# Kernel tuning notes

Hardware: AMD Instinct MI355X
Metric: run time of the kernel (lower is better)

## Reference

```python
import jax, jax.numpy as jnp
import numpy as np

N = 100000      # nodes
E = 1600000     # edges (avg degree 16)
F_IN = 128      # num_node_features
H = 128         # hidden_size
C = 64          # num_classes


def sage_conv(x, src, dst, W_l, W_r, b, num_nodes):
    """PyG SAGEConv (mean aggr): out = lin_l(mean_{j->i} x_j) + lin_r(x_i) + b."""
    msg = x[src]                                                  # [E, F] gather
    agg = jax.ops.segment_sum(msg, dst, num_segments=num_nodes)   # [N, F] scatter-add
    deg = jax.ops.segment_sum(jnp.ones((src.shape[0],), x.dtype), dst,
                              num_segments=num_nodes)             # [N]
    agg = agg / jnp.maximum(deg, 1.0)[:, None]                    # mean (safe for isolated nodes)
    return agg @ W_l + x @ W_r + b


def setup_inputs() -> dict:
    key = jax.random.key(0)
    ks = jax.random.split(key, 8)
    x = jax.random.normal(ks[0], (N, F_IN), dtype=jnp.float32)
    edge_index = jax.random.randint(ks[1], (2, E), 0, N, dtype=jnp.int32).astype(jnp.int64)
    W1_l = jax.random.normal(ks[2], (F_IN, H), dtype=jnp.float32) / np.float32(np.sqrt(F_IN))
    W1_r = jax.random.normal(ks[3], (F_IN, H), dtype=jnp.float32) / np.float32(np.sqrt(F_IN))
    b1 = jnp.zeros((H,), jnp.float32)
    W2_l = jax.random.normal(ks[4], (H, C), dtype=jnp.float32) / np.float32(np.sqrt(H))
    W2_r = jax.random.normal(ks[5], (H, C), dtype=jnp.float32) / np.float32(np.sqrt(H))
    b2 = jnp.zeros((C,), jnp.float32)
    return {"x": x, "edge_index": edge_index,
            "W1_l": W1_l, "W1_r": W1_r, "b1": b1,
            "W2_l": W2_l, "W2_r": W2_r, "b2": b2}


def reference(x, edge_index, W1_l, W1_r, b1, W2_l, W2_r, b2):
    src, dst = edge_index[0], edge_index[1]
    h = jax.nn.relu(sage_conv(x, src, dst, W1_l, W1_r, b1, N))   # dropout: eval mode => identity
    logits = sage_conv(h, src, dst, W2_l, W2_r, b2, N)
    return jax.nn.log_softmax(logits, axis=1)
```

## Files before the change

### kernel.cpp

```cpp
#include <hip/hip_runtime.h>

#define Nn 100000
#define Ee 1600000
#define FIN 128
#define HID 128
#define CLS 64
#define NB 196
#define BCAP 9216

typedef unsigned short ushort_t;
typedef unsigned char uchar_t;
typedef unsigned int uint_t;
typedef __attribute__((ext_vector_type(8))) short bf16x8;
typedef __attribute__((ext_vector_type(4))) float f32x4;
typedef __attribute__((ext_vector_type(2))) float f32x2;

__device__ __forceinline__ ushort_t f2bf(float f) {
    uint_t u = __float_as_uint(f);
    return (ushort_t)((u + 0x7fffu + ((u >> 16) & 1u)) >> 16);
}
__device__ __forceinline__ float bflo(uint_t u) { return __uint_as_float(u << 16); }
__device__ __forceinline__ float bfhi(uint_t u) { return __uint_as_float(u & 0xffff0000u); }


__global__ __launch_bounds__(1024) void k_front(const int* __restrict__ src,
                                                const int* __restrict__ dst,
                                                int* __restrict__ bcur,
                                                uint2* __restrict__ bedge,
                                                const float* __restrict__ x,
                                                ushort_t* __restrict__ xb,
                                                uint_t* __restrict__ xq,
                                                const float* __restrict__ W1l,
                                                const float* __restrict__ W1r,
                                                const float* __restrict__ W2l,
                                                const float* __restrict__ W2r,
                                                ushort_t* __restrict__ w1lt,
                                                ushort_t* __restrict__ w1rt,
                                                ushort_t* __restrict__ w2lt,
                                                ushort_t* __restrict__ w2rt) {
    __shared__ int h[NB];
    __shared__ int lbase[NB];
    int b = blockIdx.x;
    int t = threadIdx.x;
    if (b < NB) {
        if (t < NB) h[t] = 0;
        __syncthreads();
        int base = b * 8192;
        int bk[8], loc[8];
        #pragma unroll
        for (int it = 0; it < 8; ++it) {
            int e = base + it * 1024 + t;
            if (e < Ee) {
                bk[it] = dst[e] >> 9;
                loc[it] = atomicAdd(&h[bk[it]], 1);
            }
        }
        __syncthreads();
        if (t < NB && h[t]) lbase[t] = atomicAdd(&bcur[t], h[t]);
        __syncthreads();
        #pragma unroll
        for (int it = 0; it < 8; ++it) {
            int e = base + it * 1024 + t;
            if (e < Ee) {
                int pos = lbase[bk[it]] + loc[it];
                if (pos < BCAP)
                    bedge[(size_t)bk[it] * BCAP + pos] = make_uint2((uint_t)src[e], (uint_t)dst[e]);
            }
        }
    } else if (b < NB + 3125) {
        int i = (b - NB) * 1024 + t;
        float4 v = reinterpret_cast<const float4*>(x)[i];
        ushort4 o;
        o.x = f2bf(v.x); o.y = f2bf(v.y); o.z = f2bf(v.z); o.w = f2bf(v.w);
        reinterpret_cast<ushort4*>(xb)[i] = o;
        int q = __builtin_amdgcn_cvt_pk_fp8_f32(v.x, v.y, 0, false);
        q = __builtin_amdgcn_cvt_pk_fp8_f32(v.z, v.w, q, true);
        xq[i] = (uint_t)q;
    } else {
        int j = b - (NB + 3125);
        const float* Wsrc; ushort_t* Wdst; int Ncols; int cb;
        if (j < 16)      { Wsrc = W1l; Wdst = w1lt; Ncols = 128; cb = j; }
        else if (j < 32) { Wsrc = W1r; Wdst = w1rt; Ncols = 128; cb = j - 16; }
        else if (j < 40) { Wsrc = W2l; Wdst = w2lt; Ncols = 64;  cb = j - 32; }
        else             { Wsrc = W2r; Wdst = w2rt; Ncols = 64;  cb = j - 40; }
        int i = cb * 1024 + t;
        if (i < 128 * Ncols) {
            int k = i / Ncols, n = i % Ncols;
            Wdst[(size_t)n * 128 + k] = f2bf(Wsrc[i]);
        }
    }
}

__global__ __launch_bounds__(1024) void k_fillB(const uint2* __restrict__ bedge,
                                                const int* __restrict__ bcur,
                                                int* __restrict__ rowptr,
                                                int* __restrict__ csr) {
    __shared__ int h[512];
    __shared__ int off[512];
    __shared__ int sbase;
    int b = blockIdx.x, t = threadIdx.x;
    if (t < 256) off[t] = (t < NB) ? min(bcur[t], BCAP) : 0;
    __syncthreads();
    for (int o = 1; o < 256; o <<= 1) {
        int v = (t < 256 && t >= o) ? off[t - o] : 0;
        __syncthreads();
        if (t < 256) off[t] += v;
        __syncthreads();
    }
    if (t == 0) sbase = off[b] - min(bcur[b], BCAP);
    if (b == NB - 1 && t == 0) rowptr[Nn] = off[NB - 1];
    __syncthreads();
    int base_ = sbase;
    int n = min(bcur[b], BCAP);
    int node0 = b << 9;
    const uint2* be = bedge + (size_t)b * BCAP;
    if (t < 512) h[t] = 0;
    __syncthreads();
    for (int i = t; i < n; i += 1024)
        atomicAdd(&h[(int)be[i].y - node0], 1);
    __syncthreads();
    if (t < 512) off[t] = h[t];
    __syncthreads();
    for (int o = 1; o < 512; o <<= 1) {
        int v = (t < 512 && t >= o) ? off[t - o] : 0;
        __syncthreads();
        if (t < 512) off[t] += v;
        __syncthreads();
    }
    if (t < 512) {
        int excl = off[t] - h[t];
        int node = node0 + t;
        if (node < Nn) rowptr[node] = base_ + excl;
        h[t] = excl;
    }
    __syncthreads();
    for (int i = t; i < n; i += 1024) {
        uint2 ed = be[i];
        int loc = atomicAdd(&h[(int)ed.y - node0], 1);
        csr[base_ + loc] = (int)ed.x;
    }
}


__global__ __launch_bounds__(256) void k_agg1(const uchar_t* __restrict__ xq,
                                              const int* __restrict__ rowptr,
                                              const int* __restrict__ csr,
                                              ushort_t* __restrict__ outb) {
    int wid = (blockIdx.x * blockDim.x + threadIdx.x) >> 6;
    int lane = threadIdx.x & 63;
    if (wid >= Nn) return;
    int s0 = __builtin_amdgcn_readfirstlane(rowptr[wid]);
    int s1 = __builtin_amdgcn_readfirstlane(rowptr[wid + 1]);
    float ax = 0.f, ay = 0.f;
    int e = s0;
    for (; e + 16 <= s1; e += 16) {
        int idx[16];
        #pragma unroll
        for (int j = 0; j < 16; ++j) idx[j] = __builtin_amdgcn_readfirstlane(csr[e + j]);
        ushort_t u[16];
        #pragma unroll
        for (int j = 0; j < 16; ++j)
            u[j] = *reinterpret_cast<const ushort_t*>(xq + (size_t)idx[j] * 128 + lane * 2);
        #pragma unroll
        for (int j = 0; j < 16; ++j) {
            f32x2 f = __builtin_amdgcn_cvt_pk_f32_fp8((int)u[j], false);
            ax += f.x; ay += f.y;
        }
    }
    for (; e + 8 <= s1; e += 8) {
        int idx[8];
        #pragma unroll
        for (int j = 0; j < 8; ++j) idx[j] = __builtin_amdgcn_readfirstlane(csr[e + j]);
        ushort_t u[8];
        #pragma unroll
        for (int j = 0; j < 8; ++j)
            u[j] = *reinterpret_cast<const ushort_t*>(xq + (size_t)idx[j] * 128 + lane * 2);
        #pragma unroll
        for (int j = 0; j < 8; ++j) {
            f32x2 f = __builtin_amdgcn_cvt_pk_f32_fp8((int)u[j], false);
            ax += f.x; ay += f.y;
        }
    }
    for (; e < s1; ++e) {
        int s = __builtin_amdgcn_readfirstlane(csr[e]);
        ushort_t u = *reinterpret_cast<const ushort_t*>(xq + (size_t)s * 128 + lane * 2);
        f32x2 f = __builtin_amdgcn_cvt_pk_f32_fp8((int)u, false);
        ax += f.x; ay += f.y;
    }
    float invd = (s1 > s0) ? 1.0f / (float)(s1 - s0) : 0.0f;
    uint_t o = (uint_t)f2bf(ax * invd) | ((uint_t)f2bf(ay * invd) << 16);
    *reinterpret_cast<uint_t*>(outb + (size_t)wid * 128 + lane * 2) = o;
}


__global__ __launch_bounds__(512) void k_gemm1m(const ushort_t* __restrict__ Ab0,
                                                const ushort_t* __restrict__ Ab1,
                                                const ushort_t* __restrict__ Wt0,
                                                const ushort_t* __restrict__ Wt1,
                                                const float* __restrict__ bias,
                                                ushort_t* __restrict__ hb) {
    __shared__ ushort_t lw[2 * 16384];
    const int tid = threadIdx.x;
    char* lwc = reinterpret_cast<char*>(lw);
    #pragma unroll
    for (int i = 0; i < 8; ++i) {
        int c = tid + i * 512;
        int pair = c >> 11;
        int col = (c & 2047) >> 4;
        int kc = c & 15;
        const ushort_t* Wsrc = pair ? Wt1 : Wt0;
        uint4 v = *reinterpret_cast<const uint4*>(Wsrc + col * 128 + kc * 8);
        int dst = ((pair << 15) | (col << 8) | (kc << 4)) ^ ((col & 7) << 4);
        *reinterpret_cast<uint4*>(lwc + dst) = v;
    }
    __syncthreads();

    int gw = (blockIdx.x * 512 + tid) >> 6;
    int lane = tid & 63;
    if (gw >= Nn / 16) return;
    int row0 = gw * 16;
    int r = lane & 15;
    int kg = lane >> 4;
    f32x4 acc[8];
    #pragma unroll
    for (int c = 0; c < 8; ++c) acc[c] = (f32x4){0.f, 0.f, 0.f, 0.f};
    #pragma unroll
    for (int pair = 0; pair < 2; ++pair) {
        const ushort_t* A = pair ? Ab1 : Ab0;
        #pragma unroll
        for (int ks = 0; ks < 4; ++ks) {
            int kbase = ks * 32 + kg * 8;
            bf16x8 af = *reinterpret_cast<const bf16x8*>(A + (size_t)(row0 + r) * 128 + kbase);
            #pragma unroll
            for (int c = 0; c < 8; ++c) {
                int boff = ((pair << 15) | ((c * 16 + r) << 8) | (ks * 64 + kg * 16))
                           ^ ((r & 7) << 4);
                bf16x8 bf = *reinterpret_cast<const bf16x8*>(lwc + boff);
                acc[c] = __builtin_amdgcn_mfma_f32_16x16x32_bf16(af, bf, acc[c], 0, 0, 0);
            }
        }
    }
    #pragma unroll
    for (int c = 0; c < 8; ++c) {
        float bv = bias[c * 16 + r];
        #pragma unroll
        for (int i = 0; i < 4; ++i) {
            int row = row0 + kg * 4 + i;
            hb[(size_t)row * 128 + c * 16 + r] = f2bf(fmaxf(acc[c][i] + bv, 0.f));
        }
    }
}

__global__ __launch_bounds__(256) void k_gemm2f(const ushort_t* __restrict__ Ab,
                                                const ushort_t* __restrict__ Wtl,
                                                const ushort_t* __restrict__ Wtr,
                                                uchar_t* __restrict__ tb8,
                                                float* __restrict__ outu) {
    int gw = (blockIdx.x * 256 + threadIdx.x) >> 6;
    int lane = threadIdx.x & 63;
    if (gw >= Nn / 16) return;
    int row0 = gw * 16;
    int r = lane & 15;
    int kg = lane >> 4;
    f32x4 accL[4], accR[4];
    #pragma unroll
    for (int c = 0; c < 4; ++c) {
        accL[c] = (f32x4){0.f, 0.f, 0.f, 0.f};
        accR[c] = (f32x4){0.f, 0.f, 0.f, 0.f};
    }
    #pragma unroll
    for (int ks = 0; ks < 4; ++ks) {
        int kbase = ks * 32 + kg * 8;
        bf16x8 af = *reinterpret_cast<const bf16x8*>(Ab + (size_t)(row0 + r) * 128 + kbase);
        #pragma unroll
        for (int c = 0; c < 4; ++c) {
            bf16x8 bl = *reinterpret_cast<const bf16x8*>(Wtl + (size_t)(c * 16 + r) * 128 + kbase);
            accL[c] = __builtin_amdgcn_mfma_f32_16x16x32_bf16(af, bl, accL[c], 0, 0, 0);
            bf16x8 br = *reinterpret_cast<const bf16x8*>(Wtr + (size_t)(c * 16 + r) * 128 + kbase);
            accR[c] = __builtin_amdgcn_mfma_f32_16x16x32_bf16(af, br, accR[c], 0, 0, 0);
        }
    }
    #pragma unroll
    for (int c = 0; c < 4; ++c) {
        #pragma unroll
        for (int i = 0; i < 4; ++i) {
            int row = row0 + kg * 4 + i;
            int q = __builtin_amdgcn_cvt_pk_fp8_f32(accL[c][i], accL[c][i], 0, false);
            tb8[(size_t)row * 64 + c * 16 + r] = (uchar_t)(q & 0xff);
            outu[(size_t)row * 64 + c * 16 + r] = accR[c][i];
        }
    }
}


__global__ __launch_bounds__(256) void k_logsm(float* __restrict__ out,
                                               const uchar_t* __restrict__ tb8,
                                               const int* __restrict__ rowptr,
                                               const int* __restrict__ csr,
                                               const float* __restrict__ bias) {
    int wid = (blockIdx.x * blockDim.x + threadIdx.x) >> 6;
    int lane = threadIdx.x & 63;
    if (wid >= Nn) return;
    int s0 = __builtin_amdgcn_readfirstlane(rowptr[wid]);
    int s1 = __builtin_amdgcn_readfirstlane(rowptr[wid + 1]);
    float a = 0.f;
    int e = s0;
    for (; e + 16 <= s1; e += 16) {
        int idx[16];
        #pragma unroll
        for (int j = 0; j < 16; ++j) idx[j] = __builtin_amdgcn_readfirstlane(csr[e + j]);
        uchar_t u[16];
        #pragma unroll
        for (int j = 0; j < 16; ++j) u[j] = tb8[(size_t)idx[j] * 64 + lane];
        #pragma unroll
        for (int j = 0; j < 16; ++j) a += __builtin_amdgcn_cvt_f32_fp8((int)u[j], 0);
    }
    for (; e + 8 <= s1; e += 8) {
        int idx[8];
        #pragma unroll
        for (int j = 0; j < 8; ++j) idx[j] = __builtin_amdgcn_readfirstlane(csr[e + j]);
        uchar_t u[8];
        #pragma unroll
        for (int j = 0; j < 8; ++j) u[j] = tb8[(size_t)idx[j] * 64 + lane];
        #pragma unroll
        for (int j = 0; j < 8; ++j) a += __builtin_amdgcn_cvt_f32_fp8((int)u[j], 0);
    }
    for (; e < s1; ++e) {
        int s = __builtin_amdgcn_readfirstlane(csr[e]);
        a += __builtin_amdgcn_cvt_f32_fp8((int)tb8[(size_t)s * 64 + lane], 0);
    }
    float invd = (s1 > s0) ? 1.0f / (float)(s1 - s0) : 0.0f;
    size_t o = (size_t)wid * 64 + lane;
    float v = (out[o] + a * invd) + bias[lane];
    float m = v;
    #pragma unroll
    for (int off = 32; off; off >>= 1) m = fmaxf(m, __shfl_xor(m, off));
    float ex = __expf(v - m);
    float s_ = ex;
    #pragma unroll
    for (int off = 32; off; off >>= 1) s_ += __shfl_xor(s_, off);
    out[o] = v - m - __logf(s_);
}


extern "C" void kernel_launch(void* const* d_in, const int* in_sizes, int n_in,
                              void* d_out, int out_size, void* d_ws, size_t ws_size,
                              hipStream_t stream) {
    const float* x   = (const float*)d_in[0];
    const int*   ei  = (const int*)d_in[1];
    const float* W1l = (const float*)d_in[2];
    const float* W1r = (const float*)d_in[3];
    const float* b1  = (const float*)d_in[4];
    const float* W2l = (const float*)d_in[5];
    const float* W2r = (const float*)d_in[6];
    const float* b2  = (const float*)d_in[7];
    float* out = (float*)d_out;

    char* ws = (char*)d_ws;
    int*      rowptr = (int*)(ws + 800768);
    int*      csr    = (int*)(ws + 1201152);
    ushort_t* xb     = (ushort_t*)(ws + 7601152);
    ushort_t* aggb   = (ushort_t*)(ws + 33201152);
    ushort_t* w1lt   = (ushort_t*)(ws + 58801152);
    ushort_t* w1rt   = (ushort_t*)(ws + 58833920);
    ushort_t* w2lt   = (ushort_t*)(ws + 58866688);
    ushort_t* w2rt   = (ushort_t*)(ws + 58883072);
    uint2*    bedge  = (uint2*)(ws + 60000000);
    int*      bcur   = (int*)(ws + 74450688);
    uint_t*   xq     = (uint_t*)(ws + 74451968);
    ushort_t* hb     = (ushort_t*)(ws + 84401152);
    uchar_t*  tb8    = (uchar_t*)(ws + 7601152);

    const int* src = ei;
    const int* dst = ei + Ee;

    hipMemsetAsync(bcur, 0, NB * 4, stream);

    k_front<<<NB + 3125 + 48, 1024, 0, stream>>>(src, dst, bcur, bedge, x, xb, xq,
                                                 W1l, W1r, W2l, W2r,
                                                 w1lt, w1rt, w2lt, w2rt);
    k_fillB<<<NB, 1024, 0, stream>>>(bedge, bcur, rowptr, csr);

    k_agg1<<<(Nn + 3) / 4, 256, 0, stream>>>((const uchar_t*)xq, rowptr, csr, aggb);
    k_gemm1m<<<(Nn / 16 + 7) / 8, 512, 0, stream>>>(aggb, xb, w1lt, w1rt, b1, hb);

    k_gemm2f<<<(Nn / 16 + 3) / 4, 256, 0, stream>>>(hb, w2lt, w2rt, tb8, out);
    k_logsm<<<(Nn + 3) / 4, 256, 0, stream>>>(out, tb8, rowptr, csr, b2);
}
```

Measured before the change: 196.4 us.

## Overlap layer-1 root GEMM with neighbor aggregation in a merged kernel

Merges the first-layer gather/mean aggregation and the x@W1_r+b1 root GEMM into one launch using block-index ranges. The idea is to overlap memory-bound gathers with MFMA work and cut the second GEMM's K dimension in half. The GEMM partial is stored in bf16 in hb and read back by a reduced gemm1m2 that adds agg@W1_l and applies ReLU. This adds an extra bf16 rounding plus an extra read and write of hb. It also relocates workspace buffers, moving bedge to share space with aggb, and hoists the out load in logsm ahead of the gather loop with occupancy hints.

Result: slower. 240.8 us (+22.6%).

```diff
diff --git a/kernel.cpp b/kernel.cpp
--- a/kernel.cpp
+++ b/kernel.cpp
@@ -7,6 +7,8 @@
 #define CLS 64
 #define NB 196
 #define BCAP 9216
+#define AGG_NB 25000
+#define PR_NB 1563
 
 typedef unsigned short ushort_t;
 typedef unsigned char uchar_t;
@@ -142,75 +144,106 @@
 }
 
 
-__global__ __launch_bounds__(256) void k_agg1(const uchar_t* __restrict__ xq,
-                                              const int* __restrict__ rowptr,
-                                              const int* __restrict__ csr,
-                                              ushort_t* __restrict__ outb) {
-    int wid = (blockIdx.x * blockDim.x + threadIdx.x) >> 6;
-    int lane = threadIdx.x & 63;
-    if (wid >= Nn) return;
-    int s0 = __builtin_amdgcn_readfirstlane(rowptr[wid]);
-    int s1 = __builtin_amdgcn_readfirstlane(rowptr[wid + 1]);
-    float ax = 0.f, ay = 0.f;
-    int e = s0;
-    for (; e + 16 <= s1; e += 16) {
-        int idx[16];
-        #pragma unroll
-        for (int j = 0; j < 16; ++j) idx[j] = __builtin_amdgcn_readfirstlane(csr[e + j]);
-        ushort_t u[16];
-        #pragma unroll
-        for (int j = 0; j < 16; ++j)
-            u[j] = *reinterpret_cast<const ushort_t*>(xq + (size_t)idx[j] * 128 + lane * 2);
-        #pragma unroll
-        for (int j = 0; j < 16; ++j) {
-            f32x2 f = __builtin_amdgcn_cvt_pk_f32_fp8((int)u[j], false);
+__global__ __launch_bounds__(256, 8) void k_mid(const uchar_t* __restrict__ xq,
+                                                const int* __restrict__ rowptr,
+                                                const int* __restrict__ csr,
+                                                ushort_t* __restrict__ aggb,
+                                                const ushort_t* __restrict__ xb,
+                                                const ushort_t* __restrict__ w1rt,
+                                                const float* __restrict__ b1,
+                                                ushort_t* __restrict__ pr) {
+    int b = blockIdx.x;
+    int tid = threadIdx.x;
+    int lane = tid & 63;
+    if (b < AGG_NB) {
+        int wid = (b * 256 + tid) >> 6;
+        if (wid >= Nn) return;
+        int s0 = __builtin_amdgcn_readfirstlane(rowptr[wid]);
+        int s1 = __builtin_amdgcn_readfirstlane(rowptr[wid + 1]);
+        float ax = 0.f, ay = 0.f;
+        int e = s0;
+        for (; e + 16 <= s1; e += 16) {
+            int idx[16];
+            #pragma unroll
+            for (int j = 0; j < 16; ++j) idx[j] = __builtin_amdgcn_readfirstlane(csr[e + j]);
+            ushort_t u[16];
+            #pragma unroll
+            for (int j = 0; j < 16; ++j)
+                u[j] = *reinterpret_cast<const ushort_t*>(xq + (size_t)idx[j] * 128 + lane * 2);
+            #pragma unroll
+            for (int j = 0; j < 16; ++j) {
+                f32x2 f = __builtin_amdgcn_cvt_pk_f32_fp8((int)u[j], false);
+                ax += f.x; ay += f.y;
+            }
+        }
+        for (; e + 8 <= s1; e += 8) {
+            int idx[8];
+            #pragma unroll
+            for (int j = 0; j < 8; ++j) idx[j] = __builtin_amdgcn_readfirstlane(csr[e + j]);
+            ushort_t u[8];
+            #pragma unroll
+            for (int j = 0; j < 8; ++j)
+                u[j] = *reinterpret_cast<const ushort_t*>(xq + (size_t)idx[j] * 128 + lane * 2);
+            #pragma unroll
+            for (int j = 0; j < 8; ++j) {
+                f32x2 f = __builtin_amdgcn_cvt_pk_f32_fp8((int)u[j], false);
+                ax += f.x; ay += f.y;
+            }
+        }
+        for (; e < s1; ++e) {
+            int s = __builtin_amdgcn_readfirstlane(csr[e]);
+            ushort_t u = *reinterpret_cast<const ushort_t*>(xq + (size_t)s * 128 + lane * 2);
+            f32x2 f = __builtin_amdgcn_cvt_pk_f32_fp8((int)u, false);
             ax += f.x; ay += f.y;
         }
-    }
-    for (; e + 8 <= s1; e += 8) {
-        int idx[8];
-        #pragma unroll
-        for (int j = 0; j < 8; ++j) idx[j] = __builtin_amdgcn_readfirstlane(csr[e + j]);
-        ushort_t u[8];
-        #pragma unroll
-        for (int j = 0; j < 8; ++j)
-            u[j] = *reinterpret_cast<const ushort_t*>(xq + (size_t)idx[j] * 128 + lane * 2);
-        #pragma unroll
-        for (int j = 0; j < 8; ++j) {
-            f32x2 f = __builtin_amdgcn_cvt_pk_f32_fp8((int)u[j], false);
-            ax += f.x; ay += f.y;
-        }
-    }
-    for (; e < s1; ++e) {
-        int s = __builtin_amdgcn_readfirstlane(csr[e]);
-        ushort_t u = *reinterpret_cast<const ushort_t*>(xq + (size_t)s * 128 + lane * 2);
-        f32x2 f = __builtin_amdgcn_cvt_pk_f32_fp8((int)u, false);
-        ax += f.x; ay += f.y;
-    }
-    float invd = (s1 > s0) ? 1.0f / (float)(s1 - s0) : 0.0f;
-    uint_t o = (uint_t)f2bf(ax * invd) | ((uint_t)f2bf(ay * invd) << 16);
-    *reinterpret_cast<uint_t*>(outb + (size_t)wid * 128 + lane * 2) = o;
-}
-
-
-__global__ __launch_bounds__(512) void k_gemm1m(const ushort_t* __restrict__ Ab0,
-                                                const ushort_t* __restrict__ Ab1,
-                                                const ushort_t* __restrict__ Wt0,
-                                                const ushort_t* __restrict__ Wt1,
-                                                const float* __restrict__ bias,
-                                                ushort_t* __restrict__ hb) {
-    __shared__ ushort_t lw[2 * 16384];
+        float invd = (s1 > s0) ? 1.0f / (float)(s1 - s0) : 0.0f;
+        uint_t o = (uint_t)f2bf(ax * invd) | ((uint_t)f2bf(ay * invd) << 16);
+        *reinterpret_cast<uint_t*>(aggb + (size_t)wid * 128 + lane * 2) = o;
+    } else {
+        int gw = (b - AGG_NB) * 4 + (tid >> 6);
+        if (gw >= Nn / 16) return;
+        int row0 = gw * 16;
+        int r = lane & 15;
+        int kg = lane >> 4;
+        f32x4 acc[8];
+        #pragma unroll
+        for (int c = 0; c < 8; ++c) acc[c] = (f32x4){0.f, 0.f, 0.f, 0.f};
+        #pragma unroll
+        for (int ks = 0; ks < 4; ++ks) {
+            int kbase = ks * 32 + kg * 8;
+            bf16x8 af = *reinterpret_cast<const bf16x8*>(xb + (size_t)(row0 + r) * 128 + kbase);
+            #pragma unroll
+            for (int c = 0; c < 8; ++c) {
+                bf16x8 bf = *reinterpret_cast<const bf16x8*>(w1rt + (size_t)(c * 16 + r) * 128 + kbase);
+                acc[c] = __builtin_amdgcn_mfma_f32_16x16x32_bf16(af, bf, acc[c], 0, 0, 0);
+            }
+        }
+        #pragma unroll
+        for (int c = 0; c < 8; ++c) {
+            float bv = b1[c * 16 + r];
+            #pragma unroll
+            for (int i = 0; i < 4; ++i) {
+                int row = row0 + kg * 4 + i;
+                pr[(size_t)row * 128 + c * 16 + r] = f2bf(acc[c][i] + bv);
+            }
+        }
+    }
+}
+
+
+__global__ __launch_bounds__(512) void k_gemm1m2(const ushort_t* __restrict__ Ab,
+                                                 const ushort_t* __restrict__ Wt0,
+                                                 ushort_t* __restrict__ hb) {
+    __shared__ ushort_t lw[16384];
     const int tid = threadIdx.x;
     char* lwc = reinterpret_cast<char*>(lw);
     #pragma unroll
-    for (int i = 0; i < 8; ++i) {
+    for (int i = 0; i < 4; ++i) {
         int c = tid + i * 512;
-        int pair = c >> 11;
-        int col = (c & 2047) >> 4;
+        int col = c >> 4;
         int kc = c & 15;
-        const ushort_t* Wsrc = pair ? Wt1 : Wt0;
-        uint4 v = *reinterpret_cast<const uint4*>(Wsrc + col * 128 + kc * 8);
-        int dst = ((pair << 15) | (col << 8) | (kc << 4)) ^ ((col & 7) << 4);
+        uint4 v = *reinterpret_cast<const uint4*>(Wt0 + col * 128 + kc * 8);
+        int dst = ((col << 8) | (kc << 4)) ^ ((col & 7) << 4);
         *reinterpret_cast<uint4*>(lwc + dst) = v;
     }
     __syncthreads();
@@ -225,28 +258,24 @@
     #pragma unroll
     for (int c = 0; c < 8; ++c) acc[c] = (f32x4){0.f, 0.f, 0.f, 0.f};
     #pragma unroll
-    for (int pair = 0; pair < 2; ++pair) {
-        const ushort_t* A = pair ? Ab1 : Ab0;
-        #pragma unroll
-        for (int ks = 0; ks < 4; ++ks) {
-            int kbase = ks * 32 + kg * 8;
-            bf16x8 af = *reinterpret_cast<const bf16x8*>(A + (size_t)(row0 + r) * 128 + kbase);
-            #pragma unroll
-            for (int c = 0; c < 8; ++c) {
-                int boff = ((pair << 15) | ((c * 16 + r) << 8) | (ks * 64 + kg * 16))
-                           ^ ((r & 7) << 4);
-                bf16x8 bf = *reinterpret_cast<const bf16x8*>(lwc + boff);
-                acc[c] = __builtin_amdgcn_mfma_f32_16x16x32_bf16(af, bf, acc[c], 0, 0, 0);
-            }
+    for (int ks = 0; ks < 4; ++ks) {
+        int kbase = ks * 32 + kg * 8;
+        bf16x8 af = *reinterpret_cast<const bf16x8*>(Ab + (size_t)(row0 + r) * 128 + kbase);
+        #pragma unroll
+        for (int c = 0; c < 8; ++c) {
+            int boff = (((c * 16 + r) << 8) | (ks * 64 + kg * 16)) ^ ((r & 7) << 4);
+            bf16x8 bf = *reinterpret_cast<const bf16x8*>(lwc + boff);
+            acc[c] = __builtin_amdgcn_mfma_f32_16x16x32_bf16(af, bf, acc[c], 0, 0, 0);
         }
     }
     #pragma unroll
     for (int c = 0; c < 8; ++c) {
-        float bv = bias[c * 16 + r];
         #pragma unroll
         for (int i = 0; i < 4; ++i) {
             int row = row0 + kg * 4 + i;
-            hb[(size_t)row * 128 + c * 16 + r] = f2bf(fmaxf(acc[c][i] + bv, 0.f));
+            size_t o = (size_t)row * 128 + c * 16 + r;
+            float prv = __uint_as_float(((uint_t)hb[o]) << 16);
+            hb[o] = f2bf(fmaxf(acc[c][i] + prv, 0.f));
         }
     }
 }
@@ -293,16 +322,18 @@
 }
 
 
-__global__ __launch_bounds__(256) void k_logsm(float* __restrict__ out,
-                                               const uchar_t* __restrict__ tb8,
-                                               const int* __restrict__ rowptr,
-                                               const int* __restrict__ csr,
-                                               const float* __restrict__ bias) {
+__global__ __launch_bounds__(256, 8) void k_logsm(float* __restrict__ out,
+                                                  const uchar_t* __restrict__ tb8,
+                                                  const int* __restrict__ rowptr,
+                                                  const int* __restrict__ csr,
+                                                  const float* __restrict__ bias) {
     int wid = (blockIdx.x * blockDim.x + threadIdx.x) >> 6;
     int lane = threadIdx.x & 63;
     if (wid >= Nn) return;
     int s0 = __builtin_amdgcn_readfirstlane(rowptr[wid]);
     int s1 = __builtin_amdgcn_readfirstlane(rowptr[wid + 1]);
+    size_t o = (size_t)wid * 64 + lane;
+    float uval = out[o];
     float a = 0.f;
     int e = s0;
     for (; e + 16 <= s1; e += 16) {
@@ -330,8 +361,7 @@
         a += __builtin_amdgcn_cvt_f32_fp8((int)tb8[(size_t)s * 64 + lane], 0);
     }
     float invd = (s1 > s0) ? 1.0f / (float)(s1 - s0) : 0.0f;
-    size_t o = (size_t)wid * 64 + lane;
-    float v = (out[o] + a * invd) + bias[lane];
+    float v = (uval + a * invd) + bias[lane];
     float m = v;
     #pragma unroll
     for (int off = 32; off; off >>= 1) m = fmaxf(m, __shfl_xor(m, off));
@@ -360,14 +390,14 @@
     int*      rowptr = (int*)(ws + 800768);
     int*      csr    = (int*)(ws + 1201152);
     ushort_t* xb     = (ushort_t*)(ws + 7601152);
+    uint2*    bedge  = (uint2*)(ws + 33201152);
+    int*      bcur   = (int*)(ws + 47651840);
     ushort_t* aggb   = (ushort_t*)(ws + 33201152);
     ushort_t* w1lt   = (ushort_t*)(ws + 58801152);
     ushort_t* w1rt   = (ushort_t*)(ws + 58833920);
     ushort_t* w2lt   = (ushort_t*)(ws + 58866688);
     ushort_t* w2rt   = (ushort_t*)(ws + 58883072);
-    uint2*    bedge  = (uint2*)(ws + 60000000);
-    int*      bcur   = (int*)(ws + 74450688);
-    uint_t*   xq     = (uint_t*)(ws + 74451968);
+    uint_t*   xq     = (uint_t*)(ws + 60000000);
     ushort_t* hb     = (ushort_t*)(ws + 84401152);
     uchar_t*  tb8    = (uchar_t*)(ws + 7601152);
 
@@ -381,8 +411,9 @@
                                                  w1lt, w1rt, w2lt, w2rt);
     k_fillB<<<NB, 1024, 0, stream>>>(bedge, bcur, rowptr, csr);
 
-    k_agg1<<<(Nn + 3) / 4, 256, 0, stream>>>((const uchar_t*)xq, rowptr, csr, aggb);
-    k_gemm1m<<<(Nn / 16 + 7) / 8, 512, 0, stream>>>(aggb, xb, w1lt, w1rt, b1, hb);
+    k_mid<<<AGG_NB + PR_NB, 256, 0, stream>>>((const uchar_t*)xq, rowptr, csr, aggb,
+                                              xb, w1rt, b1, hb);
+    k_gemm1m2<<<(Nn / 16 + 7) / 8, 512, 0, stream>>>(aggb, w1lt, hb);
 
     k_gemm2f<<<(Nn / 16 + 3) / 4, 256, 0, stream>>>(hb, w2lt, w2rt, tb8, out);
     k_logsm<<<(Nn + 3) / 4, 256, 0, stream>>>(out, tb8, rowptr, csr, b2);
```

## Fuse layer-1 and layer-2 GEMMs, keeping hidden activations in LDS

Applied to the files above, without the earlier changes.

Merges the first-layer GEMM (with bias and ReLU) and the second-layer dual GEMM into one kernel. The bf16 hidden tile for each wave is written to swizzled shared memory and read back as the A operand for the second GEMM, so the hidden activation no longer goes to global memory. This removes one kernel launch and the write and re-read of the 100000x128 hidden buffer. In exchange it adds two block barriers, keeps all waves resident for the barrier, and reuses the weight LDS region. The fp8 output buffer also moves to a new workspace offset.

Result: faster. 191.3 us (-2.6%).

```diff
diff --git a/kernel.cpp b/kernel.cpp
--- a/kernel.cpp
+++ b/kernel.cpp
@@ -193,15 +193,17 @@
 }
 
 
-__global__ __launch_bounds__(512) void k_gemm1m(const ushort_t* __restrict__ Ab0,
+__global__ __launch_bounds__(512) void k_gemm12(const ushort_t* __restrict__ Ab0,
                                                 const ushort_t* __restrict__ Ab1,
                                                 const ushort_t* __restrict__ Wt0,
                                                 const ushort_t* __restrict__ Wt1,
-                                                const float* __restrict__ bias,
-                                                ushort_t* __restrict__ hb) {
-    __shared__ ushort_t lw[2 * 16384];
+                                                const float* __restrict__ b1,
+                                                const ushort_t* __restrict__ Wtl,
+                                                const ushort_t* __restrict__ Wtr,
+                                                uchar_t* __restrict__ tb8,
+                                                float* __restrict__ outu) {
+    __shared__ char lwc[2 * 32768];
     const int tid = threadIdx.x;
-    char* lwc = reinterpret_cast<char*>(lw);
     #pragma unroll
     for (int i = 0; i < 8; ++i) {
         int c = tid + i * 512;
@@ -215,53 +217,52 @@
     }
     __syncthreads();
 
-    int gw = (blockIdx.x * 512 + tid) >> 6;
+    int wid = tid >> 6;
+    int gw = blockIdx.x * 8 + wid;
     int lane = tid & 63;
-    if (gw >= Nn / 16) return;
-    int row0 = gw * 16;
     int r = lane & 15;
     int kg = lane >> 4;
+    bool active = (gw < Nn / 16);
+    int row0 = gw * 16;
+
     f32x4 acc[8];
     #pragma unroll
     for (int c = 0; c < 8; ++c) acc[c] = (f32x4){0.f, 0.f, 0.f, 0.f};
-    #pragma unroll
-    for (int pair = 0; pair < 2; ++pair) {
-        const ushort_t* A = pair ? Ab1 : Ab0;
-        #pragma unroll
-        for (int ks = 0; ks < 4; ++ks) {
-            int kbase = ks * 32 + kg * 8;
-            bf16x8 af = *reinterpret_cast<const bf16x8*>(A + (size_t)(row0 + r) * 128 + kbase);
+    if (active) {
+        #pragma unroll
+        for (int pair = 0; pair < 2; ++pair) {
+            const ushort_t* A = pair ? Ab1 : Ab0;
             #pragma unroll
-            for (int c = 0; c < 8; ++c) {
-                int boff = ((pair << 15) | ((c * 16 + r) << 8) | (ks * 64 + kg * 16))
-                           ^ ((r & 7) << 4);
-                bf16x8 bf = *reinterpret_cast<const bf16x8*>(lwc + boff);
-                acc[c] = __builtin_amdgcn_mfma_f32_16x16x32_bf16(af, bf, acc[c], 0, 0, 0);
+            for (int ks = 0; ks < 4; ++ks) {
+                int kbase = ks * 32 + kg * 8;
+                bf16x8 af = *reinterpret_cast<const bf16x8*>(A + (size_t)(row0 + r) * 128 + kbase);
+                #pragma unroll
+                for (int c = 0; c < 8; ++c) {
+                    int boff = ((pair << 15) | ((c * 16 + r) << 8) | (ks * 64 + kg * 16))
+                               ^ ((r & 7) << 4);
+                    bf16x8 bf = *reinterpret_cast<const bf16x8*>(lwc + boff);
+                    acc[c] = __builtin_amdgcn_mfma_f32_16x16x32_bf16(af, bf, acc[c], 0, 0, 0);
+                }
             }
         }
     }
-    #pragma unroll
-    for (int c = 0; c < 8; ++c) {
-        float bv = bias[c * 16 + r];
-        #pragma unroll
-        for (int i = 0; i < 4; ++i) {
-            int row = row0 + kg * 4 + i;
-            hb[(size_t)row * 128 + c * 16 + r] = f2bf(fmaxf(acc[c][i] + bv, 0.f));
-        }
-    }
-}
-
-__global__ __launch_bounds__(256) void k_gemm2f(const ushort_t* __restrict__ Ab,
-                                                const ushort_t* __restrict__ Wtl,
-                                                const ushort_t* __restrict__ Wtr,
-                                                uchar_t* __restrict__ tb8,
-                                                float* __restrict__ outu) {
-    int gw = (blockIdx.x * 256 + threadIdx.x) >> 6;
-    int lane = threadIdx.x & 63;
-    if (gw >= Nn / 16) return;
-    int row0 = gw * 16;
-    int r = lane & 15;
-    int kg = lane >> 4;
+    __syncthreads();
+
+    if (active) {
+        #pragma unroll
+        for (int c = 0; c < 8; ++c) {
+            float bv = b1[c * 16 + r];
+            #pragma unroll
+            for (int i = 0; i < 4; ++i) {
+                int rl = wid * 16 + kg * 4 + i;
+                int ha = ((rl << 8) | ((c * 16 + r) << 1)) ^ ((rl & 7) << 4);
+                *reinterpret_cast<ushort_t*>(lwc + ha) = f2bf(fmaxf(acc[c][i] + bv, 0.f));
+            }
+        }
+    }
+    __syncthreads();
+    if (!active) return;
+
     f32x4 accL[4], accR[4];
     #pragma unroll
     for (int c = 0; c < 4; ++c) {
@@ -271,7 +272,9 @@
     #pragma unroll
     for (int ks = 0; ks < 4; ++ks) {
         int kbase = ks * 32 + kg * 8;
-        bf16x8 af = *reinterpret_cast<const bf16x8*>(Ab + (size_t)(row0 + r) * 128 + kbase);
+        int rl = wid * 16 + r;
+        int ra = ((rl << 8) | (kbase << 1)) ^ ((r & 7) << 4);
+        bf16x8 af = *reinterpret_cast<const bf16x8*>(lwc + ra);
         #pragma unroll
         for (int c = 0; c < 4; ++c) {
             bf16x8 bl = *reinterpret_cast<const bf16x8*>(Wtl + (size_t)(c * 16 + r) * 128 + kbase);
@@ -368,8 +371,7 @@
     uint2*    bedge  = (uint2*)(ws + 60000000);
     int*      bcur   = (int*)(ws + 74450688);
     uint_t*   xq     = (uint_t*)(ws + 74451968);
-    ushort_t* hb     = (ushort_t*)(ws + 84401152);
-    uchar_t*  tb8    = (uchar_t*)(ws + 7601152);
+    uchar_t*  tb8    = (uchar_t*)(ws + 87252992);
 
     const int* src = ei;
     const int* dst = ei + Ee;
@@ -382,8 +384,9 @@
     k_fillB<<<NB, 1024, 0, stream>>>(bedge, bcur, rowptr, csr);
 
     k_agg1<<<(Nn + 3) / 4, 256, 0, stream>>>((const uchar_t*)xq, rowptr, csr, aggb);
-    k_gemm1m<<<(Nn / 16 + 7) / 8, 512, 0, stream>>>(aggb, xb, w1lt, w1rt, b1, hb);
-
-    k_gemm2f<<<(Nn / 16 + 3) / 4, 256, 0, stream>>>(hb, w2lt, w2rt, tb8, out);
+
+    k_gemm12<<<(Nn / 16 + 7) / 8, 512, 0, stream>>>(aggb, xb, w1lt, w1rt, b1,
+                                                    w2lt, w2rt, tb8, out);
+
     k_logsm<<<(Nn + 3) / 4, 256, 0, stream>>>(out, tb8, rowptr, csr, b2);
 }
```
